# Performance work log

Hardware: AMD Instinct MI355X
Metric: run time of the kernel (lower is better)

## Reference

```python
import jax, jax.numpy as jnp
import numpy as np

B, C, H, W = 4, 512, 64, 64
CH = C // 2  # 256


def setup_inputs() -> dict:
    key = jax.random.key(0)
    ks = jax.random.split(key, 10)
    s = 0.02  # keep logits in sane range for softmax
    return {
        "Fc": jax.random.normal(ks[0], (B, C, H, W), jnp.float32),
        "Fs": jax.random.normal(ks[1], (B, C, H, W), jnp.float32),
        "f_w": jax.random.normal(ks[2], (CH, C), jnp.float32) * s,
        "f_b": jax.random.normal(ks[3], (CH,), jnp.float32) * s,
        "g_w": jax.random.normal(ks[4], (CH, C), jnp.float32) * s,
        "g_b": jax.random.normal(ks[5], (CH,), jnp.float32) * s,
        "h_w": jax.random.normal(ks[6], (C, C), jnp.float32) * s,
        "h_b": jax.random.normal(ks[7], (C,), jnp.float32) * s,
        "out_w": jax.random.normal(ks[8], (C, C), jnp.float32) * s,
        "out_b": jax.random.normal(ks[9], (C,), jnp.float32) * s,
    }


def _conv1x1(x, w, b):
    # x: [B,C,H,W], w: [O,C], b: [O] -> [B,O,H,W]
    return jnp.einsum('oc,bchw->bohw', w, x) + b[None, :, None, None]


def reference(Fc, Fs, f_w, f_b, g_w, g_b, h_w, h_b, out_w, out_b):
    b, c, h, w = Fc.shape
    hw = h * w
    Ff = _conv1x1(Fc, f_w, f_b).reshape(b, -1, hw)   # [B, C/2, HW]
    Fg = _conv1x1(Fs, g_w, g_b).reshape(b, -1, hw)   # [B, C/2, HW]
    Fh = _conv1x1(Fs, h_w, h_b).reshape(b, -1, hw)   # [B, C,   HW]
    d_k = Ff.shape[1]  # channels//2, matches torch d_k after permute
    # Attention[b,i,j] over style positions j
    logits = jnp.einsum('bci,bcj->bij', Ff, Fg) / jnp.sqrt(jnp.float32(d_k))
    attn = jax.nn.softmax(logits, axis=-1)           # [B, HW, HW]
    # Out[b,c,i] = sum_j Fh[b,c,j] * attn[b,i,j]
    out = jnp.einsum('bcj,bij->bci', Fh, attn).reshape(b, c, h, w)
    return _conv1x1(out, out_w, out_b) + Fc
```

## Files before the change

### kernel.cpp

```cpp
#include <hip/hip_runtime.h>
#include <hip/hip_bf16.h>

#define HW    4096
#define CDIM  512
#define CHALF 256
#define NB    4
#define FLASH_LDS 82944
#define MERGE_LDS 66048

using bf16 = __hip_bfloat16;
typedef __attribute__((ext_vector_type(8))) short short8;
typedef __attribute__((ext_vector_type(4))) float float4v;

typedef __attribute__((address_space(1))) void gvoid_t;
typedef __attribute__((address_space(3))) void svoid_t;
#define GLD16(gp, lp) \
    __builtin_amdgcn_global_load_lds((gvoid_t*)(gp), (svoid_t*)(lp), 16, 0, 0)
#define MFMA(a, b, c) __builtin_amdgcn_mfma_f32_16x16x32_bf16(a, b, c, 0, 0, 0)

static __device__ __forceinline__ short8 ld_short8(const bf16* p) {
    return *reinterpret_cast<const short8*>(p);
}
static __device__ __forceinline__ float b2f(short s) {
    unsigned u = ((unsigned)(unsigned short)s) << 16;
    return __builtin_bit_cast(float, u);
}
static __device__ __forceinline__ short f2bs(float f) {
    bf16 h = __float2bfloat16(f);
    return __builtin_bit_cast(short, h);
}

__global__ void transpose_cast(const float* __restrict__ Fc,
                               const float* __restrict__ Fs,
                               bf16* __restrict__ FcT, bf16* __restrict__ FsT) {
    __shared__ float tile[32][33];
    int p0 = blockIdx.x * 32, c0 = blockIdx.y * 32;
    int z = blockIdx.z;
    int b = z & 3, which = z >> 2;
    const float* src = (which ? Fs : Fc) + (size_t)b * CDIM * HW;
    bf16* dst = (which ? FsT : FcT) + (size_t)b * HW * CDIM;
    int tx = threadIdx.x, ty = threadIdx.y;
    for (int i = 0; i < 4; i++)
        tile[ty + 8 * i][tx] = src[(size_t)(c0 + ty + 8 * i) * HW + p0 + tx];
    __syncthreads();
    for (int i = 0; i < 4; i++)
        dst[(size_t)(p0 + ty + 8 * i) * CDIM + c0 + tx] =
            __float2bfloat16(tile[tx][ty + 8 * i]);
}

__global__ void cast4(const float* __restrict__ fw, const float* __restrict__ gw,
                      const float* __restrict__ hw, const float* __restrict__ ow,
                      bf16* __restrict__ dst) {
    int i = blockIdx.x * 256 + threadIdx.x;
    float v;
    if (i < 131072)       v = fw[i] * 0.0625f;
    else if (i < 262144)  v = gw[i - 131072];
    else if (i < 524288)  v = hw[i - 262144];
    else                  v = ow[i - 524288];
    dst[i] = __float2bfloat16(v);
}

__launch_bounds__(256, 2)
__global__ void gemm_fg(const bf16* __restrict__ A1, const bf16* __restrict__ A2,
                        size_t sA,
                        const bf16* __restrict__ W1, const bf16* __restrict__ W2,
                        const float* __restrict__ b1, const float* __restrict__ b2,
                        float bs1, float bs2,
                        bf16* __restrict__ D1, bf16* __restrict__ D2, size_t sD,
                        int zhalf, int N, int K) {
    __shared__ bf16 Asf[2][8192];
    __shared__ bf16 Bsf[2][8192];
    int lid = blockIdx.x;
    int xcd = lid & 7, idx = lid >> 3;
    int bx = idx & 1;
    int yzg = xcd * 32 + (idx >> 1);
    int z = yzg >> 5;
    int by = yzg & 31;
    const bf16 *A, *W; const float* bias; float bsc; bf16* D;
    if (z < zhalf) { A = A1 + sA * z;           W = W1; bias = b1; bsc = bs1; D = D1 + sD * z; }
    else           { A = A2 + sA * (z - zhalf); W = W2; bias = b2; bsc = bs2; D = D2 + sD * (z - zhalf); }
    int m0 = by * 128, n0 = bx * 128;
    int t = threadIdx.x;
    int w = t >> 6, lane = t & 63;
    int wm = w >> 1, wn = w & 1;
    int l15 = lane & 15, quad = lane >> 4;
    int lr = lane >> 3, lc = (lane & 7) ^ lr;
    int nk = K >> 6;
    float4v acc[4][4] = {};

    for (int q = 0; q < 4; q++) {
        int rb = w * 32 + q * 8;
        GLD16(A + (size_t)(m0 + rb + lr) * K + lc * 8, &Asf[0][rb * 64]);
        GLD16(W + (size_t)(n0 + rb + lr) * K + lc * 8, &Bsf[0][rb * 64]);
    }
    for (int i = 0; i < nk; i++) {
        __syncthreads();
        if (i + 1 < nk) {
            int k0 = (i + 1) << 6, nb = (i + 1) & 1;
            for (int q = 0; q < 4; q++) {
                int rb = w * 32 + q * 8;
                GLD16(A + (size_t)(m0 + rb + lr) * K + k0 + lc * 8, &Asf[nb][rb * 64]);
                GLD16(W + (size_t)(n0 + rb + lr) * K + k0 + lc * 8, &Bsf[nb][rb * 64]);
            }
        }
        int cb = i & 1;
        for (int h = 0; h < 2; h++) {
            int p = (h * 4 + quad) ^ (l15 & 7);
            short8 af[4], bfr[4];
            for (int sm = 0; sm < 4; sm++)
                af[sm] = *(const short8*)&Asf[cb][(wm * 64 + sm * 16 + l15) * 64 + p * 8];
            for (int sn = 0; sn < 4; sn++)
                bfr[sn] = *(const short8*)&Bsf[cb][(wn * 64 + sn * 16 + l15) * 64 + p * 8];
            for (int sm = 0; sm < 4; sm++)
                for (int sn = 0; sn < 4; sn++)
                    acc[sm][sn] = MFMA(af[sm], bfr[sn], acc[sm][sn]);
        }
    }
    for (int sm = 0; sm < 4; sm++)
        for (int sn = 0; sn < 4; sn++) {
            int n = n0 + wn * 64 + sn * 16 + l15;
            for (int r = 0; r < 4; r++) {
                int m = m0 + wm * 64 + sm * 16 + quad * 4 + r;
                D[(size_t)m * N + n] = __float2bfloat16(acc[sm][sn][r] + bias[n] * bsc);
            }
        }
}

__launch_bounds__(256, 2)
__global__ void gemm_bw(const bf16* __restrict__ Aw,
                        const bf16* __restrict__ Bact, size_t sB,
                        const float* __restrict__ bias,
                        bf16* __restrict__ Dp, size_t sD,
                        int N, int K) {
    __shared__ bf16 Asf[2][8192];
    __shared__ bf16 Bsf[2][8192];
    int lid = blockIdx.x;
    int xcd = lid & 7, idx = lid >> 3;
    int my = idx & 3;
    int nzg = xcd * 16 + (idx >> 2);
    int z = nzg >> 5;
    int nx = nzg & 31;
    const bf16* A = Aw;
    const bf16* Bm = Bact + sB * z;
    int m0 = my * 128, n0 = nx * 128;
    int t = threadIdx.x;
    int w = t >> 6, lane = t & 63;
    int wm = w >> 1, wn = w & 1;
    int l15 = lane & 15, quad = lane >> 4;
    int lr = lane >> 3, lc = (lane & 7) ^ lr;
    int nk = K >> 6;
    float4v acc[4][4] = {};

    for (int q = 0; q < 4; q++) {
        int rb = w * 32 + q * 8;
        GLD16(A + (size_t)(m0 + rb + lr) * K + lc * 8, &Asf[0][rb * 64]);
        GLD16(Bm + (size_t)(n0 + rb + lr) * K + lc * 8, &Bsf[0][rb * 64]);
    }
    for (int i = 0; i < nk; i++) {
        __syncthreads();
        if (i + 1 < nk) {
            int k0 = (i + 1) << 6, nb = (i + 1) & 1;
            for (int q = 0; q < 4; q++) {
                int rb = w * 32 + q * 8;
                GLD16(A + (size_t)(m0 + rb + lr) * K + k0 + lc * 8, &Asf[nb][rb * 64]);
                GLD16(Bm + (size_t)(n0 + rb + lr) * K + k0 + lc * 8, &Bsf[nb][rb * 64]);
            }
        }
        int cb = i & 1;
        for (int h = 0; h < 2; h++) {
            int p = (h * 4 + quad) ^ (l15 & 7);
            short8 af[4], bfr[4];
            for (int sm = 0; sm < 4; sm++)
                af[sm] = *(const short8*)&Asf[cb][(wm * 64 + sm * 16 + l15) * 64 + p * 8];
            for (int sn = 0; sn < 4; sn++)
                bfr[sn] = *(const short8*)&Bsf[cb][(wn * 64 + sn * 16 + l15) * 64 + p * 8];
            for (int sm = 0; sm < 4; sm++)
                for (int sn = 0; sn < 4; sn++)
                    acc[sm][sn] = MFMA(af[sm], bfr[sn], acc[sm][sn]);
        }
    }
    for (int sm = 0; sm < 4; sm++)
        for (int sn = 0; sn < 4; sn++) {
            int n = n0 + wn * 64 + sn * 16 + l15;
            for (int r = 0; r < 4; r++) {
                int m = m0 + wm * 64 + sm * 16 + quad * 4 + r;
                Dp[sD * z + (size_t)m * N + n] =
                    __float2bfloat16(acc[sm][sn][r] + bias[m]);
            }
        }
}

__launch_bounds__(512, 1)
__global__ void flash_attn(const bf16* __restrict__ Q_, const bf16* __restrict__ Kt_,
                           const bf16* __restrict__ V_,
                           bf16* __restrict__ O0_, bf16* __restrict__ O1_,
                           float* __restrict__ L0_, float* __restrict__ L1_) {
    extern __shared__ char smem[];
    bf16* Ksf = (bf16*)smem;
    short* Ps = (short*)(smem + 65536);
    float* lpart = (float*)(smem + 81920);

    int lid = blockIdx.x;
    int stream = lid & 7;
    int b = stream & 3, jh = stream >> 2;
    int i0 = (lid >> 3) * 128;
    const bf16* Kt = Kt_ + (size_t)b * HW * CHALF;
    const bf16* V  = V_ + (size_t)b * CDIM * HW;
    bf16* Out   = (jh ? O1_ : O0_) + ((size_t)b * HW + i0) * CDIM;
    float* Lout = (jh ? L1_ : L0_) + (size_t)b * HW + i0;

    int t = threadIdx.x;
    int w = t >> 6, lane = t & 63;
    int l15 = lane & 15, quad = lane >> 4;
    int rm   = (w & 3) * 32;
    int cnw  = (w >> 2) * 32;
    int chb  = (w >> 2) * 4;
    int c0w  = w * 64;
    int jbeg = jh * (HW / 2), jend = jbeg + HW / 2;

    short8 qf0[8], qf1[8];
    {
        const bf16* qp = Q_ + ((size_t)b * HW + i0 + rm + l15) * CHALF + quad * 8;
        #pragma unroll
        for (int k8 = 0; k8 < 8; k8++) {
            qf0[k8] = ld_short8(qp + k8 * 32);
            qf1[k8] = ld_short8(qp + 16 * CHALF + k8 * 32);
        }
    }
    {
        int r0 = lane >> 5, cc = lane & 31;
        for (int i = 0; i < 4; i++) {
            int rp = i * 8 + w;
            int r = 2 * rp + r0;
            int c = cc ^ (r & 7);
            GLD16(Kt + (size_t)(jbeg + r) * CHALF + c * 8, &Ksf[rp * 512]);
        }
    }
    float l_lane[2][4] = {};
    float4v oacc[8][4] = {};
    __syncthreads();

    const bf16* vp = V + (size_t)(c0w + l15) * HW + quad * 8;
    int cb = 0;
    for (int j0 = jbeg; j0 < jend; j0 += 64) {
        short8 va[4];
        #pragma unroll
        for (int sn = 0; sn < 4; sn++)
            va[sn] = ld_short8(vp + j0 + (size_t)(sn * 16) * HW);
        if (j0 + 64 < jend) {
            int r0 = lane >> 5, cc = lane & 31;
            for (int i = 0; i < 4; i++) {
                int rp = i * 8 + w;
                int r = 2 * rp + r0;
                int c = cc ^ (r & 7);
                GLD16(Kt + (size_t)(j0 + 64 + r) * CHALF + c * 8,
                      &Ksf[(cb ^ 1) * 16384 + rp * 512]);
            }
        }
        const bf16* Kb = Ksf + cb * 16384;
        float4v s00 = {}, s01 = {}, s10 = {}, s11 = {};
        __builtin_amdgcn_s_setprio(1);
        #pragma unroll
        for (int k8 = 0; k8 < 8; k8++) {
            int pq = ((k8 * 4 + quad) ^ (l15 & 7)) * 8;
            short8 k0 = *(const short8*)&Kb[(cnw + l15) * 256 + pq];
            short8 k1 = *(const short8*)&Kb[(cnw + 16 + l15) * 256 + pq];
            s00 = MFMA(qf0[k8], k0, s00);
            s01 = MFMA(qf0[k8], k1, s01);
            s10 = MFMA(qf1[k8], k0, s10);
            s11 = MFMA(qf1[k8], k1, s11);
        }
        __builtin_amdgcn_s_setprio(0);
        #pragma unroll
        for (int r = 0; r < 4; r++) {
            int rl0 = rm + quad * 4 + r, rl1 = rl0 + 16;
            int cw = chb + (l15 >> 3);
            float p00 = __expf(s00[r]);
            float p01 = __expf(s01[r]);
            float p10 = __expf(s10[r]);
            float p11 = __expf(s11[r]);
            l_lane[0][r] += p00 + p01;
            l_lane[1][r] += p10 + p11;
            Ps[rl0 * 64 + ((cw + rl0) & 7) * 8 + (l15 & 7)]     = f2bs(p00);
            Ps[rl0 * 64 + ((cw + 2 + rl0) & 7) * 8 + (l15 & 7)] = f2bs(p01);
            Ps[rl1 * 64 + ((cw + rl1) & 7) * 8 + (l15 & 7)]     = f2bs(p10);
            Ps[rl1 * 64 + ((cw + 2 + rl1) & 7) * 8 + (l15 & 7)] = f2bs(p11);
        }
        asm volatile("s_waitcnt lgkmcnt(0)" ::: "memory");
        __builtin_amdgcn_s_barrier();
        __builtin_amdgcn_s_setprio(1);
        #pragma unroll
        for (int sm = 0; sm < 8; sm++) {
            int rl = sm * 16 + l15;
            short8 pf = *(const short8*)&Ps[rl * 64 + ((quad + rl) & 7) * 8];
            #pragma unroll
            for (int sn = 0; sn < 4; sn++)
                oacc[sm][sn] = MFMA(pf, va[sn], oacc[sm][sn]);
        }
        __builtin_amdgcn_s_setprio(0);
        short8 vb[4];
        #pragma unroll
        for (int sn = 0; sn < 4; sn++)
            vb[sn] = ld_short8(vp + j0 + 32 + (size_t)(sn * 16) * HW);
        __builtin_amdgcn_s_setprio(1);
        #pragma unroll
        for (int sm = 0; sm < 8; sm++) {
            int rl = sm * 16 + l15;
            short8 pf = *(const short8*)&Ps[rl * 64 + ((4 + quad + rl) & 7) * 8];
            #pragma unroll
            for (int sn = 0; sn < 4; sn++)
                oacc[sm][sn] = MFMA(pf, vb[sn], oacc[sm][sn]);
        }
        __builtin_amdgcn_s_setprio(0);
        asm volatile("s_waitcnt vmcnt(0) lgkmcnt(0)" ::: "memory");
        __builtin_amdgcn_s_barrier();
        cb ^= 1;
    }

    #pragma unroll
    for (int ms = 0; ms < 2; ms++)
        for (int r = 0; r < 4; r++) {
            float red = l_lane[ms][r];
            red += __shfl_xor(red, 1);
            red += __shfl_xor(red, 2);
            red += __shfl_xor(red, 4);
            red += __shfl_xor(red, 8);
            if (l15 == 0)
                lpart[(w >> 2) * 128 + rm + ms * 16 + quad * 4 + r] = red;
        }
    __syncthreads();
    if ((w >> 2) == 0 && l15 == 0)
        for (int ms = 0; ms < 2; ms++)
            for (int r = 0; r < 4; r++) {
                int rl = rm + ms * 16 + quad * 4 + r;
                Lout[rl] = lpart[rl] + lpart[128 + rl];
            }
    for (int sm = 0; sm < 8; sm++)
        for (int r = 0; r < 4; r++) {
            int rl = sm * 16 + quad * 4 + r;
            float li = 1.0f / (lpart[rl] + lpart[128 + rl]);
            for (int sn = 0; sn < 4; sn++)
                Out[(size_t)rl * CDIM + c0w + sn * 16 + l15] =
                    __float2bfloat16(oacc[sm][sn][r] * li);
        }
}

__launch_bounds__(256, 1)
__global__ void merge_out(const bf16* __restrict__ Op0, const bf16* __restrict__ Op1,
                          const float* __restrict__ L0, const float* __restrict__ L1,
                          const bf16* __restrict__ ow, const float* __restrict__ out_b,
                          const float* __restrict__ Fc, float* __restrict__ out) {
    extern __shared__ char smem[];
    short* Os = (short*)smem;
    float* lw = (float*)(smem + 65536);

    int rt = blockIdx.x;
    int b = rt >> 6;
    int i0 = (rt & 63) * 64;
    size_t obase = ((size_t)b * HW + i0) * CDIM;
    int t = threadIdx.x;

    if (t < 64) {
        float l0 = L0[(size_t)b * HW + i0 + t];
        float l1 = L1[(size_t)b * HW + i0 + t];
        float inv = 1.f / (l0 + l1);
        lw[t * 2] = l0 * inv;
        lw[t * 2 + 1] = l1 * inv;
    }
    __syncthreads();

    for (int q = 0; q < 16; q++) {
        int idx = q * 256 + t;
        int row = idx >> 6, cc = idx & 63;
        short8 a = ld_short8(Op0 + obase + (size_t)row * CDIM + cc * 8);
        short8 c = ld_short8(Op1 + obase + (size_t)row * CDIM + cc * 8);
        float w0 = lw[row * 2], w1 = lw[row * 2 + 1];
        short8 o;
        #pragma unroll
        for (int j = 0; j < 8; j++)
            o[j] = f2bs(w0 * b2f(a[j]) + w1 * b2f(c[j]));
        *(short8*)&Os[row * 512 + (cc ^ (row & 7)) * 8] = o;
    }
    __syncthreads();

    int w = t >> 6, lane = t & 63;
    int l15 = lane & 15, quad = lane >> 4;
    int m0 = w * 128;
    float4v acc[8][4] = {};
    for (int k8 = 0; k8 < 16; k8++) {
        short8 bfr[4];
        #pragma unroll
        for (int n16 = 0; n16 < 4; n16++)
            bfr[n16] = *(const short8*)&Os[(n16 * 16 + l15) * 512 +
                (((k8 * 4 + quad) ^ (l15 & 7))) * 8];
        short8 af[8];
        #pragma unroll
        for (int m16 = 0; m16 < 8; m16++)
            af[m16] = ld_short8(ow + (size_t)(m0 + m16 * 16 + l15) * CDIM +
                                k8 * 32 + quad * 8);
        #pragma unroll
        for (int m16 = 0; m16 < 8; m16++)
            for (int n16 = 0; n16 < 4; n16++)
                acc[m16][n16] = MFMA(af[m16], bfr[n16], acc[m16][n16]);
    }

    const float* fcb = Fc + (size_t)b * CDIM * HW;
    float* outb = out + (size_t)b * CDIM * HW;
    for (int m16 = 0; m16 < 8; m16++)
        for (int r = 0; r < 4; r++) {
            int co = m0 + m16 * 16 + quad * 4 + r;
            float bb = out_b[co];
            for (int n16 = 0; n16 < 4; n16++) {
                int i = i0 + n16 * 16 + l15;
                outb[(size_t)co * HW + i] =
                    acc[m16][n16][r] + bb + fcb[(size_t)co * HW + i];
            }
        }
}

extern "C" void kernel_launch(void* const* d_in, const int* in_sizes, int n_in,
                              void* d_out, int out_size, void* d_ws, size_t ws_size,
                              hipStream_t stream) {
    const float* Fc   = (const float*)d_in[0];
    const float* Fs   = (const float*)d_in[1];
    const float* f_w  = (const float*)d_in[2];
    const float* f_b  = (const float*)d_in[3];
    const float* g_w  = (const float*)d_in[4];
    const float* g_b  = (const float*)d_in[5];
    const float* h_w  = (const float*)d_in[6];
    const float* h_b  = (const float*)d_in[7];
    const float* out_w = (const float*)d_in[8];
    const float* out_b = (const float*)d_in[9];
    float* out = (float*)d_out;

    bf16* FcT = (bf16*)d_ws;
    bf16* FsT = FcT + (size_t)NB * HW * CDIM;
    bf16* FfT = FsT + (size_t)NB * HW * CDIM;
    bf16* FgT = FfT + (size_t)NB * HW * CHALF;
    bf16* Fh  = FgT + (size_t)NB * HW * CHALF;
    bf16* fw  = Fh  + (size_t)NB * CDIM * HW;
    bf16* gw  = fw + (size_t)CHALF * CDIM;
    bf16* hw  = gw + (size_t)CHALF * CDIM;
    bf16* ow  = hw + (size_t)CDIM * CDIM;
    float* L0 = (float*)(ow + (size_t)CDIM * CDIM);
    float* L1 = L0 + (size_t)NB * HW;
    bf16* Op0 = FcT;
    bf16* Op1 = FsT;

    hipFuncSetAttribute((const void*)flash_attn,
                        hipFuncAttributeMaxDynamicSharedMemorySize, FLASH_LDS);
    hipFuncSetAttribute((const void*)merge_out,
                        hipFuncAttributeMaxDynamicSharedMemorySize, MERGE_LDS);

    transpose_cast<<<dim3(HW / 32, CDIM / 32, NB * 2), dim3(32, 8), 0, stream>>>(
        Fc, Fs, FcT, FsT);
    cast4<<<dim3(786432 / 256), 256, 0, stream>>>(f_w, g_w, h_w, out_w, fw);

    gemm_fg<<<dim3(512), 256, 0, stream>>>(
        FcT, FsT, (size_t)HW * CDIM, fw, gw, f_b, g_b, 0.0625f, 1.0f,
        FfT, FgT, (size_t)HW * CHALF, NB, CHALF, CDIM);
    gemm_bw<<<dim3(512), 256, 0, stream>>>(
        hw, FsT, (size_t)HW * CDIM, h_b, Fh, (size_t)CDIM * HW, HW, CDIM);
    flash_attn<<<dim3(256), 512, FLASH_LDS, stream>>>(
        FfT, FgT, Fh, Op0, Op1, L0, L1);
    merge_out<<<dim3(256), 256, MERGE_LDS, stream>>>(
        Op0, Op1, L0, L1, ow, out_b, Fc, out);
}
```

Measured before the change: 404.4 us.

## Software-pipeline flash attention: overlap PV of previous tile with QK of next

```diff
diff --git a/kernel.cpp b/kernel.cpp
--- a/kernel.cpp
+++ b/kernel.cpp
@@ -5,7 +5,7 @@
 #define CDIM  512
 #define CHALF 256
 #define NB    4
-#define FLASH_LDS 82944
+#define FLASH_LDS 99328
 #define MERGE_LDS 66048
 
 using bf16 = __hip_bfloat16;
@@ -198,7 +198,7 @@
     extern __shared__ char smem[];
     bf16* Ksf = (bf16*)smem;
     short* Ps = (short*)(smem + 65536);
-    float* lpart = (float*)(smem + 81920);
+    float* lpart = (float*)(smem + 98304);
 
     int lid = blockIdx.x;
     int stream = lid & 7;
@@ -227,37 +227,25 @@
             qf1[k8] = ld_short8(qp + 16 * CHALF + k8 * 32);
         }
     }
-    {
-        int r0 = lane >> 5, cc = lane & 31;
-        for (int i = 0; i < 4; i++) {
-            int rp = i * 8 + w;
-            int r = 2 * rp + r0;
-            int c = cc ^ (r & 7);
-            GLD16(Kt + (size_t)(jbeg + r) * CHALF + c * 8, &Ksf[rp * 512]);
-        }
+    int r0 = lane >> 5, cc = lane & 31;
+
+    for (int i = 0; i < 4; i++) {
+        int rp = i * 8 + w;
+        int r = 2 * rp + r0;
+        int c = cc ^ (r & 7);
+        GLD16(Kt + (size_t)(jbeg + r) * CHALF + c * 8, &Ksf[rp * 512]);
     }
     float l_lane[2][4] = {};
     float4v oacc[8][4] = {};
-    __syncthreads();
+    asm volatile("s_waitcnt vmcnt(0)" ::: "memory");
+    __builtin_amdgcn_s_barrier();
 
     const bf16* vp = V + (size_t)(c0w + l15) * HW + quad * 8;
-    int cb = 0;
-    for (int j0 = jbeg; j0 < jend; j0 += 64) {
-        short8 va[4];
-        #pragma unroll
-        for (int sn = 0; sn < 4; sn++)
-            va[sn] = ld_short8(vp + j0 + (size_t)(sn * 16) * HW);
-        if (j0 + 64 < jend) {
-            int r0 = lane >> 5, cc = lane & 31;
-            for (int i = 0; i < 4; i++) {
-                int rp = i * 8 + w;
-                int r = 2 * rp + r0;
-                int c = cc ^ (r & 7);
-                GLD16(Kt + (size_t)(j0 + 64 + r) * CHALF + c * 8,
-                      &Ksf[(cb ^ 1) * 16384 + rp * 512]);
-            }
-        }
-        const bf16* Kb = Ksf + cb * 16384;
+    short8 va[4];
+
+    auto qksm = [&](int kb) {
+        const bf16* Kb = Ksf + kb * 16384;
+        short* Pb = Ps + kb * 8192;
         float4v s00 = {}, s01 = {}, s10 = {}, s11 = {};
         __builtin_amdgcn_s_setprio(1);
         #pragma unroll
@@ -281,40 +269,77 @@
             float p11 = __expf(s11[r]);
             l_lane[0][r] += p00 + p01;
             l_lane[1][r] += p10 + p11;
-            Ps[rl0 * 64 + ((cw + rl0) & 7) * 8 + (l15 & 7)]     = f2bs(p00);
-            Ps[rl0 * 64 + ((cw + 2 + rl0) & 7) * 8 + (l15 & 7)] = f2bs(p01);
-            Ps[rl1 * 64 + ((cw + rl1) & 7) * 8 + (l15 & 7)]     = f2bs(p10);
-            Ps[rl1 * 64 + ((cw + 2 + rl1) & 7) * 8 + (l15 & 7)] = f2bs(p11);
-        }
-        asm volatile("s_waitcnt lgkmcnt(0)" ::: "memory");
-        __builtin_amdgcn_s_barrier();
+            Pb[rl0 * 64 + ((cw + rl0) & 7) * 8 + (l15 & 7)]     = f2bs(p00);
+            Pb[rl0 * 64 + ((cw + 2 + rl0) & 7) * 8 + (l15 & 7)] = f2bs(p01);
+            Pb[rl1 * 64 + ((cw + rl1) & 7) * 8 + (l15 & 7)]     = f2bs(p10);
+            Pb[rl1 * 64 + ((cw + 2 + rl1) & 7) * 8 + (l15 & 7)] = f2bs(p11);
+        }
+    };
+    auto pvhalf = [&](int pb, int coff, const short8* vv) {
         __builtin_amdgcn_s_setprio(1);
         #pragma unroll
         for (int sm = 0; sm < 8; sm++) {
             int rl = sm * 16 + l15;
-            short8 pf = *(const short8*)&Ps[rl * 64 + ((quad + rl) & 7) * 8];
+            short8 pf = *(const short8*)&Ps[pb * 8192 + rl * 64 +
+                                            ((coff + quad + rl) & 7) * 8];
             #pragma unroll
             for (int sn = 0; sn < 4; sn++)
-                oacc[sm][sn] = MFMA(pf, va[sn], oacc[sm][sn]);
+                oacc[sm][sn] = MFMA(pf, vv[sn], oacc[sm][sn]);
         }
         __builtin_amdgcn_s_setprio(0);
+    };
+
+    for (int i = 0; i < 4; i++) {
+        int rp = i * 8 + w;
+        int r = 2 * rp + r0;
+        int c = cc ^ (r & 7);
+        GLD16(Kt + (size_t)(jbeg + 64 + r) * CHALF + c * 8,
+              &Ksf[16384 + rp * 512]);
+    }
+    #pragma unroll
+    for (int sn = 0; sn < 4; sn++)
+        va[sn] = ld_short8(vp + jbeg + (size_t)(sn * 16) * HW);
+    qksm(0);
+    asm volatile("s_waitcnt lgkmcnt(0)" ::: "memory");
+    asm volatile("s_waitcnt vmcnt(4)" ::: "memory");
+    __builtin_amdgcn_s_barrier();
+
+    for (int it = 1; it < 32; it++) {
+        int j0 = jbeg + it * 64, jp = j0 - 64;
+        int pb = (it - 1) & 1, kb = it & 1;
         short8 vb[4];
         #pragma unroll
         for (int sn = 0; sn < 4; sn++)
-            vb[sn] = ld_short8(vp + j0 + 32 + (size_t)(sn * 16) * HW);
-        __builtin_amdgcn_s_setprio(1);
-        #pragma unroll
-        for (int sm = 0; sm < 8; sm++) {
-            int rl = sm * 16 + l15;
-            short8 pf = *(const short8*)&Ps[rl * 64 + ((4 + quad + rl) & 7) * 8];
-            #pragma unroll
-            for (int sn = 0; sn < 4; sn++)
-                oacc[sm][sn] = MFMA(pf, vb[sn], oacc[sm][sn]);
-        }
-        __builtin_amdgcn_s_setprio(0);
-        asm volatile("s_waitcnt vmcnt(0) lgkmcnt(0)" ::: "memory");
+            vb[sn] = ld_short8(vp + jp + 32 + (size_t)(sn * 16) * HW);
+        if (it < 31) {
+            for (int i = 0; i < 4; i++) {
+                int rp = i * 8 + w;
+                int r = 2 * rp + r0;
+                int c = cc ^ (r & 7);
+                GLD16(Kt + (size_t)(j0 + 64 + r) * CHALF + c * 8,
+                      &Ksf[(kb ^ 1) * 16384 + rp * 512]);
+            }
+        }
+        pvhalf(pb, 0, va);
+        __builtin_amdgcn_sched_barrier(0);
+        #pragma unroll
+        for (int sn = 0; sn < 4; sn++)
+            va[sn] = ld_short8(vp + j0 + (size_t)(sn * 16) * HW);
+        pvhalf(pb, 4, vb);
+        qksm(kb);
+        asm volatile("s_waitcnt lgkmcnt(0)" ::: "memory");
+        asm volatile("s_waitcnt vmcnt(4)" ::: "memory");
         __builtin_amdgcn_s_barrier();
-        cb ^= 1;
+    }
+
+    {
+        short8 vb[4];
+        int jp = jend - 64;
+        #pragma unroll
+        for (int sn = 0; sn < 4; sn++)
+            vb[sn] = ld_short8(vp + jp + 32 + (size_t)(sn * 16) * HW);
+        pvhalf(1, 0, va);
+        pvhalf(1, 4, vb);
     }
 
     #pragma unroll
```

New measurement: 370.9 us. -8.3%, faster.

## Restructure flash attention to 16 waves with software-pipelined QK and PV stages

Applied to the files above, without the earlier changes.

```diff
diff --git a/kernel.cpp b/kernel.cpp
--- a/kernel.cpp
+++ b/kernel.cpp
@@ -5,7 +5,7 @@
 #define CDIM  512
 #define CHALF 256
 #define NB    4
-#define FLASH_LDS 82944
+#define FLASH_LDS 132096
 #define MERGE_LDS 66048
 
 using bf16 = __hip_bfloat16;
@@ -190,15 +190,16 @@
         }
 }
 
-__launch_bounds__(512, 1)
+__launch_bounds__(1024)
 __global__ void flash_attn(const bf16* __restrict__ Q_, const bf16* __restrict__ Kt_,
                            const bf16* __restrict__ V_,
                            bf16* __restrict__ O0_, bf16* __restrict__ O1_,
                            float* __restrict__ L0_, float* __restrict__ L1_) {
     extern __shared__ char smem[];
-    bf16* Ksf = (bf16*)smem;
-    short* Ps = (short*)(smem + 65536);
-    float* lpart = (float*)(smem + 81920);
+    bf16* Qs  = (bf16*)smem;
+    bf16* Ksf = (bf16*)(smem + 65536);
+    short* Ps = (short*)(smem + 98304);
+    float* lpart = (float*)(smem + 131072);
 
     int lid = blockIdx.x;
     int stream = lid & 7;
@@ -212,132 +213,119 @@
     int t = threadIdx.x;
     int w = t >> 6, lane = t & 63;
     int l15 = lane & 15, quad = lane >> 4;
-    int rm   = (w & 3) * 32;
-    int cnw  = (w >> 2) * 32;
-    int chb  = (w >> 2) * 4;
-    int c0w  = w * 64;
-    int jbeg = jh * (HW / 2), jend = jbeg + HW / 2;
-
-    short8 qf0[8], qf1[8];
-    {
-        const bf16* qp = Q_ + ((size_t)b * HW + i0 + rm + l15) * CHALF + quad * 8;
-        #pragma unroll
-        for (int k8 = 0; k8 < 8; k8++) {
-            qf0[k8] = ld_short8(qp + k8 * 32);
-            qf1[k8] = ld_short8(qp + 16 * CHALF + k8 * 32);
-        }
-    }
-    {
-        int r0 = lane >> 5, cc = lane & 31;
-        for (int i = 0; i < 4; i++) {
-            int rp = i * 8 + w;
-            int r = 2 * rp + r0;
-            int c = cc ^ (r & 7);
-            GLD16(Kt + (size_t)(jbeg + r) * CHALF + c * 8, &Ksf[rp * 512]);
-        }
-    }
-    float l_lane[2][4] = {};
-    float4v oacc[8][4] = {};
-    __syncthreads();
+    int rg  = w & 7;
+    int cg  = w >> 3;
+    int ih  = w >> 3;
+    int c0w = (w & 7) * 64;
+    int jbeg = jh * (HW / 2);
+
+    int r0 = lane >> 5, cc = lane & 31;
+
+    for (int i = 0; i < 4; i++) {
+        int rp = i * 16 + w;
+        int r = 2 * rp + r0;
+        int c = cc ^ (r & 7);
+        GLD16(Q_ + ((size_t)b * HW + i0 + r) * CHALF + c * 8, &Qs[rp * 512]);
+    }
+    for (int i = 0; i < 2; i++) {
+        int rp = i * 16 + w;
+        int r = 2 * rp + r0;
+        int c = cc ^ (r & 7);
+        GLD16(Kt + (size_t)(jbeg + r) * CHALF + c * 8, &Ksf[rp * 512]);
+    }
+    float l_lane[4] = {};
+    float4v oacc[4][4] = {};
+    asm volatile("s_waitcnt vmcnt(0)" ::: "memory");
+    __builtin_amdgcn_s_barrier();
 
     const bf16* vp = V + (size_t)(c0w + l15) * HW + quad * 8;
-    int cb = 0;
-    for (int j0 = jbeg; j0 < jend; j0 += 64) {
-        short8 va[4];
-        #pragma unroll
-        for (int sn = 0; sn < 4; sn++)
-            va[sn] = ld_short8(vp + j0 + (size_t)(sn * 16) * HW);
-        if (j0 + 64 < jend) {
-            int r0 = lane >> 5, cc = lane & 31;
-            for (int i = 0; i < 4; i++) {
-                int rp = i * 8 + w;
-                int r = 2 * rp + r0;
-                int c = cc ^ (r & 7);
-                GLD16(Kt + (size_t)(j0 + 64 + r) * CHALF + c * 8,
-                      &Ksf[(cb ^ 1) * 16384 + rp * 512]);
-            }
-        }
-        const bf16* Kb = Ksf + cb * 16384;
-        float4v s00 = {}, s01 = {}, s10 = {}, s11 = {};
+
+    auto qksm = [&](int pb) {
+        float4v s0 = {}, s1 = {};
         __builtin_amdgcn_s_setprio(1);
         #pragma unroll
         for (int k8 = 0; k8 < 8; k8++) {
             int pq = ((k8 * 4 + quad) ^ (l15 & 7)) * 8;
-            short8 k0 = *(const short8*)&Kb[(cnw + l15) * 256 + pq];
-            short8 k1 = *(const short8*)&Kb[(cnw + 16 + l15) * 256 + pq];
-            s00 = MFMA(qf0[k8], k0, s00);
-            s01 = MFMA(qf0[k8], k1, s01);
-            s10 = MFMA(qf1[k8], k0, s10);
-            s11 = MFMA(qf1[k8], k1, s11);
+            short8 qf = *(const short8*)&Qs[(rg * 16 + l15) * 256 + pq];
+            short8 k0 = *(const short8*)&Ksf[(cg * 32 + l15) * 256 + pq];
+            short8 k1 = *(const short8*)&Ksf[(cg * 32 + 16 + l15) * 256 + pq];
+            s0 = MFMA(qf, k0, s0);
+            s1 = MFMA(qf, k1, s1);
         }
         __builtin_amdgcn_s_setprio(0);
+        short* Pb = Ps + pb * 8192;
+        int cw = cg * 4 + (l15 >> 3);
         #pragma unroll
         for (int r = 0; r < 4; r++) {
-            int rl0 = rm + quad * 4 + r, rl1 = rl0 + 16;
-            int cw = chb + (l15 >> 3);
-            float p00 = __expf(s00[r]);
-            float p01 = __expf(s01[r]);
-            float p10 = __expf(s10[r]);
-            float p11 = __expf(s11[r]);
-            l_lane[0][r] += p00 + p01;
-            l_lane[1][r] += p10 + p11;
-            Ps[rl0 * 64 + ((cw + rl0) & 7) * 8 + (l15 & 7)]     = f2bs(p00);
-            Ps[rl0 * 64 + ((cw + 2 + rl0) & 7) * 8 + (l15 & 7)] = f2bs(p01);
-            Ps[rl1 * 64 + ((cw + rl1) & 7) * 8 + (l15 & 7)]     = f2bs(p10);
-            Ps[rl1 * 64 + ((cw + 2 + rl1) & 7) * 8 + (l15 & 7)] = f2bs(p11);
-        }
-        asm volatile("s_waitcnt lgkmcnt(0)" ::: "memory");
-        __builtin_amdgcn_s_barrier();
+            int rl = rg * 16 + quad * 4 + r;
+            float p0 = __expf(s0[r]);
+            float p1 = __expf(s1[r]);
+            l_lane[r] += p0 + p1;
+            Pb[rl * 64 + ((cw + rl) & 7) * 8 + (l15 & 7)]     = f2bs(p0);
+            Pb[rl * 64 + ((cw + 2 + rl) & 7) * 8 + (l15 & 7)] = f2bs(p1);
+        }
+    };
+    auto pvhalf = [&](int pb, int h, int j0) {
+        short8 va[4];
+        #pragma unroll
+        for (int sn = 0; sn < 4; sn++)
+            va[sn] = ld_short8(vp + j0 + h * 32 + (size_t)(sn * 16) * HW);
         __builtin_amdgcn_s_setprio(1);
         #pragma unroll
-        for (int sm = 0; sm < 8; sm++) {
-            int rl = sm * 16 + l15;
-            short8 pf = *(const short8*)&Ps[rl * 64 + ((quad + rl) & 7) * 8];
+        for (int sm = 0; sm < 4; sm++) {
+            int rl = ih * 64 + sm * 16 + l15;
+            short8 pf = *(const short8*)&Ps[pb * 8192 + rl * 64 +
+                                            ((h * 4 + quad + rl) & 7) * 8];
             #pragma unroll
             for (int sn = 0; sn < 4; sn++)
                 oacc[sm][sn] = MFMA(pf, va[sn], oacc[sm][sn]);
         }
         __builtin_amdgcn_s_setprio(0);
-        short8 vb[4];
-        #pragma unroll
-        for (int sn = 0; sn < 4; sn++)
-            vb[sn] = ld_short8(vp + j0 + 32 + (size_t)(sn * 16) * HW);
-        __builtin_amdgcn_s_setprio(1);
-        #pragma unroll
-        for (int sm = 0; sm < 8; sm++) {
-            int rl = sm * 16 + l15;
-            short8 pf = *(const short8*)&Ps[rl * 64 + ((4 + quad + rl) & 7) * 8];
-            #pragma unroll
-            for (int sn = 0; sn < 4; sn++)
-                oacc[sm][sn] = MFMA(pf, vb[sn], oacc[sm][sn]);
-        }
-        __builtin_amdgcn_s_setprio(0);
-        asm volatile("s_waitcnt vmcnt(0) lgkmcnt(0)" ::: "memory");
+    };
+
+    qksm(0);
+    asm volatile("s_waitcnt lgkmcnt(0)" ::: "memory");
+    __builtin_amdgcn_s_barrier();
+
+    for (int it = 1; it < 32; it++) {
+        int jp = jbeg + (it - 1) * 64;
+        for (int i = 0; i < 2; i++) {
+            int rp = i * 16 + w;
+            int r = 2 * rp + r0;
+            int c = cc ^ (r & 7);
+            GLD16(Kt + (size_t)(jbeg + it * 64 + r) * CHALF + c * 8,
+                  &Ksf[rp * 512]);
+        }
+        int pb = (it - 1) & 1;
+        pvhalf(pb, 0, jp);
+        pvhalf(pb, 1, jp);
+        asm volatile("s_waitcnt vmcnt(0)" ::: "memory");
+        qksm(it & 1);
+        asm volatile("s_waitcnt lgkmcnt(0)" ::: "memory");
         __builtin_amdgcn_s_barrier();
-        cb ^= 1;
+    }
+    {
+        int jp = jbeg + 31 * 64;
+        pvhalf(1, 0, jp);
+        pvhalf(1, 1, jp);
     }
 
     #pragma unroll
-    for (int ms = 0; ms < 2; ms++)
+    for (int r = 0; r < 4; r++) {
+        float red = l_lane[r];
+        red += __shfl_xor(red, 1);
+        red += __shfl_xor(red, 2);
+        red += __shfl_xor(red, 4);
+        red += __shfl_xor(red, 8);
+        if (l15 == 0)
+            lpart[cg * 128 + rg * 16 + quad * 4 + r] = red;
+    }
+    __syncthreads();
+    if (t < 128)
+        Lout[t] = lpart[t] + lpart[128 + t];
+    for (int sm = 0; sm < 4; sm++)
         for (int r = 0; r < 4; r++) {
-            float red = l_lane[ms][r];
-            red += __shfl_xor(red, 1);
-            red += __shfl_xor(red, 2);
-            red += __shfl_xor(red, 4);
-            red += __shfl_xor(red, 8);
-            if (l15 == 0)
-                lpart[(w >> 2) * 128 + rm + ms * 16 + quad * 4 + r] = red;
-        }
-    __syncthreads();
-    if ((w >> 2) == 0 && l15 == 0)
-        for (int ms = 0; ms < 2; ms++)
-            for (int r = 0; r < 4; r++) {
-                int rl = rm + ms * 16 + quad * 4 + r;
-                Lout[rl] = lpart[rl] + lpart[128 + rl];
-            }
-    for (int sm = 0; sm < 8; sm++)
-        for (int r = 0; r < 4; r++) {
-            int rl = sm * 16 + quad * 4 + r;
+            int rl = ih * 64 + sm * 16 + quad * 4 + r;
             float li = 1.0f / (lpart[rl] + lpart[128 + rl]);
             for (int sn = 0; sn < 4; sn++)
                 Out[(size_t)rl * CDIM + c0w + sn * 16 + l15] =
@@ -461,7 +449,7 @@
         FfT, FgT, (size_t)HW * CHALF, NB, CHALF, CDIM);
     gemm_bw<<<dim3(512), 256, 0, stream>>>(
         hw, FsT, (size_t)HW * CDIM, h_b, Fh, (size_t)CDIM * HW, HW, CDIM);
-    flash_attn<<<dim3(256), 512, FLASH_LDS, stream>>>(
+    flash_attn<<<dim3(256), 1024, FLASH_LDS, stream>>>(
         FfT, FgT, Fh, Op0, Op1, L0, L1);
     merge_out<<<dim3(256), 256, MERGE_LDS, stream>>>(
         Op0, Op1, L0, L1, ow, out_b, Fc, out);
```

After: 401.6 us. Within noise of the previous version (-0.7%).
